# Kernel optimization log

Hardware: AMD Instinct MI355X
Metric: run time of the kernel (lower is better)

Reference implementation:

```python
import jax, jax.numpy as jnp
import numpy as np

B = 65536
N_SPARSE = 20
N_VARLEN = 3
SEQ_LEN = 50
VOCAB = 100000
N_DENSE = 13


def setup_inputs() -> dict:
    key = jax.random.key(0)
    k1, k2, k3, k4, k5, k6 = jax.random.split(key, 6)
    sparse_ids = jax.random.randint(k1, (B, N_SPARSE), 0, VOCAB, dtype=jnp.int64 if jax.config.jax_enable_x64 else jnp.int32)
    varlen_ids = jax.random.randint(k2, (B, N_VARLEN, SEQ_LEN), 0, VOCAB, dtype=sparse_ids.dtype)
    dense_x = jax.random.normal(k3, (B, N_DENSE), dtype=jnp.float32)
    # dim-1 embedding table per feature, stacked: [n_feat, vocab]
    sparse_tables = jax.random.normal(k4, (N_SPARSE, VOCAB), dtype=jnp.float32)
    varlen_tables = jax.random.normal(k5, (N_VARLEN, VOCAB), dtype=jnp.float32)
    dense_w = jax.random.normal(k6, (N_DENSE,), dtype=jnp.float32) * 1e-4
    return {
        "sparse_ids": sparse_ids,
        "varlen_ids": varlen_ids,
        "dense_x": dense_x,
        "sparse_tables": sparse_tables,
        "varlen_tables": varlen_tables,
        "dense_w": dense_w,
    }


def reference(sparse_ids, varlen_ids, dense_x, sparse_tables, varlen_tables, dense_w):
    # per-feature dim-1 embedding gather for single-value sparse feats: [B, Fs]
    fs = jnp.arange(N_SPARSE)
    sparse_vals = sparse_tables[fs[None, :], sparse_ids]
    # varlen gather: [B, Fv, L]; mask_zero=True -> id 0 contributes nothing; sum pooling
    fv = jnp.arange(N_VARLEN)
    varlen_vals = varlen_tables[fv[None, :, None], varlen_ids]
    mask = (varlen_ids != 0).astype(varlen_vals.dtype)
    varlen_pool = jnp.sum(varlen_vals * mask, axis=-1)  # [B, Fv]
    # reduce_sum over concat([sparse_vals, varlen_pool]) == sum of both sums
    logit = jnp.sum(sparse_vals, axis=-1) + jnp.sum(varlen_pool, axis=-1)
    # linear dense logit: concat(dense) @ W[:,1], squeezed
    logit = logit + dense_x @ dense_w
    return logit  # [B]
```

## Files before the change

kernel.cpp:

```cpp
#include <hip/hip_runtime.h>

constexpr int B        = 65536;
constexpr int N_SPARSE = 20;
constexpr int N_VARLEN = 3;
constexpr int SEQ_LEN  = 50;
constexpr int VOCAB    = 100000;
constexpr int N_DENSE  = 13;
constexpr int VAR_TOT  = N_VARLEN * SEQ_LEN;

typedef int   v4i __attribute__((ext_vector_type(4)));
typedef float v2f __attribute__((ext_vector_type(2)));

__global__ __launch_bounds__(256) void logit_kernel(
    const int*   __restrict__ sparse_ids,
    const int*   __restrict__ varlen_ids,
    const float* __restrict__ dense_x,
    const float* __restrict__ sparse_tables,
    const float* __restrict__ varlen_tables,
    const float* __restrict__ dense_w,
    float*       __restrict__ out)
{
    const int tid = blockIdx.x * blockDim.x + threadIdx.x;
    const int g   = tid >> 4;
    const int t   = tid & 15;

    const v4i* vptr = (const v4i*)varlen_ids + (long)g * 75;
    const v4i* sptr = (const v4i*)sparse_ids + (long)g * 10;
    const v2f* dptr = (const v2f*)dense_x    + (long)g * 13;

    v4i vid[5];
    #pragma unroll
    for (int k = 0; k < 4; ++k)
        vid[k] = __builtin_nontemporal_load(vptr + (t + 16 * k));
    vid[4] = __builtin_nontemporal_load(vptr + (t > 10 ? 74 : t + 64));
    const v4i sid = __builtin_nontemporal_load(sptr + (t > 9 ? 9 : t));
    const v2f dx  = __builtin_nontemporal_load(dptr + (t > 12 ? 12 : t));

    float vval[20];
    #pragma unroll
    for (int k = 0; k < 5; ++k) {
        const int c = (k == 4) ? (t + 64) : (t + 16 * k);
        #pragma unroll
        for (int j = 0; j < 4; ++j) {
            const int s = 4 * c + j;
            int p = (s >= VAR_TOT) ? (s - VAR_TOT) : s;
            p = (p > VAR_TOT - 1) ? (VAR_TOT - 1) : p;
            const int v = (p >= 100) ? 2 : (p >= 50 ? 1 : 0);
            vval[4 * k + j] = varlen_tables[v * VOCAB + vid[k][j]];
        }
    }
    float sval[4];
    {
        const int c = (t > 9) ? 9 : t;
        #pragma unroll
        for (int j = 0; j < 4; ++j) {
            const int s = 4 * c + j;
            const int f = (s >= N_SPARSE) ? (s - N_SPARSE) : s;
            sval[j] = sparse_tables[f * VOCAB + sid[j]];
        }
    }

    float acc0 = 0.f, acc1 = 0.f;

    #pragma unroll
    for (int k = 0; k < 5; ++k) {
        const int c = (k == 4) ? (t + 64) : (t + 16 * k);
        #pragma unroll
        for (int j = 0; j < 4; ++j) {
            const int s   = 4 * c + j;
            const bool ok = (s < 2 * VAR_TOT);
            const bool r1 = (s >= VAR_TOT);
            const float m = (ok && vid[k][j] != 0) ? vval[4 * k + j] : 0.f;
            acc0 += r1 ? 0.f : m;
            acc1 += r1 ? m   : 0.f;
        }
    }
    {
        const int c   = (t > 9) ? 9 : t;
        const bool ok = (t < 10);
        #pragma unroll
        for (int j = 0; j < 4; ++j) {
            const int s   = 4 * c + j;
            const bool r1 = (s >= N_SPARSE);
            const float m = ok ? sval[j] : 0.f;
            acc0 += r1 ? 0.f : m;
            acc1 += r1 ? m   : 0.f;
        }
    }
    {
        const int c   = (t > 12) ? 12 : t;
        const bool ok = (t < 13);
        #pragma unroll
        for (int j = 0; j < 2; ++j) {
            const int s   = 2 * c + j;
            const bool r1 = (s >= N_DENSE);
            const int d   = r1 ? (s - N_DENSE) : s;
            const float m = ok ? dx[j] * dense_w[d] : 0.f;
            acc0 += r1 ? 0.f : m;
            acc1 += r1 ? m   : 0.f;
        }
    }

    #pragma unroll
    for (int o = 1; o < 16; o <<= 1) {
        acc0 += __shfl_xor(acc0, o);
        acc1 += __shfl_xor(acc1, o);
    }
    if (t == 0) {
        v2f r = { acc0, acc1 };
        __builtin_nontemporal_store(r, (v2f*)out + g);
    }
}

extern "C" void kernel_launch(void* const* d_in, const int* in_sizes, int n_in,
                              void* d_out, int out_size, void* d_ws, size_t ws_size,
                              hipStream_t stream) {
    const int*   sparse_ids    = (const int*)d_in[0];
    const int*   varlen_ids    = (const int*)d_in[1];
    const float* dense_x       = (const float*)d_in[2];
    const float* sparse_tables = (const float*)d_in[3];
    const float* varlen_tables = (const float*)d_in[4];
    const float* dense_w       = (const float*)d_in[5];
    float*       out           = (float*)d_out;

    const int threads = 256;
    const int total   = (B / 2) * 16;
    const int blocks  = total / threads;
    logit_kernel<<<blocks, threads, 0, stream>>>(
        sparse_ids, varlen_ids, dense_x, sparse_tables, varlen_tables, dense_w, out);
}
```

Before: 144.3 us.

## Stage fp16 varlen tables through LDS in vocab slices instead of global gathers

```diff
diff --git a/kernel.cpp b/kernel.cpp
--- a/kernel.cpp
+++ b/kernel.cpp
@@ -8,47 +8,50 @@
 constexpr int N_DENSE  = 13;
 constexpr int VAR_TOT  = N_VARLEN * SEQ_LEN;
 
+constexpr int SLICE = 10000;
+constexpr int NPASS = VOCAB / SLICE;
+constexpr int LROW  = SLICE + 2;
+
 typedef int   v4i __attribute__((ext_vector_type(4)));
 typedef float v2f __attribute__((ext_vector_type(2)));
 
-__global__ __launch_bounds__(256) void logit_kernel(
+__global__ __launch_bounds__(512) void convert_kernel(
+    const float* __restrict__ vt, unsigned int* __restrict__ vt16)
+{
+    const int i = blockIdx.x * 512 + threadIdx.x;
+    if (i >= (N_VARLEN * VOCAB) / 2) return;
+    const v2f f = ((const v2f*)vt)[i];
+    const unsigned short lo = __builtin_bit_cast(unsigned short, (_Float16)f.x);
+    const unsigned short hi = __builtin_bit_cast(unsigned short, (_Float16)f.y);
+    vt16[i] = ((unsigned int)hi << 16) | lo;
+}
+
+__global__ __launch_bounds__(1024) void logit_kernel(
     const int*   __restrict__ sparse_ids,
     const int*   __restrict__ varlen_ids,
     const float* __restrict__ dense_x,
     const float* __restrict__ sparse_tables,
-    const float* __restrict__ varlen_tables,
     const float* __restrict__ dense_w,
+    const unsigned int* __restrict__ vt16,
     float*       __restrict__ out)
 {
-    const int tid = blockIdx.x * blockDim.x + threadIdx.x;
-    const int g   = tid >> 4;
-    const int t   = tid & 15;
+    __shared__ unsigned int ldsw[N_VARLEN * (LROW / 2)];
+    const unsigned short* lds16 = (const unsigned short*)ldsw;
+
+    const int tidb = threadIdx.x;
+    const int gtid = blockIdx.x * 1024 + tidb;
+    const int g    = gtid >> 4;
+    const int t    = gtid & 15;
 
     const v4i* vptr = (const v4i*)varlen_ids + (long)g * 75;
-    const v4i* sptr = (const v4i*)sparse_ids + (long)g * 10;
-    const v2f* dptr = (const v2f*)dense_x    + (long)g * 13;
-
     v4i vid[5];
     #pragma unroll
     for (int k = 0; k < 4; ++k)
         vid[k] = __builtin_nontemporal_load(vptr + (t + 16 * k));
     vid[4] = __builtin_nontemporal_load(vptr + (t > 10 ? 74 : t + 64));
-    const v4i sid = __builtin_nontemporal_load(sptr + (t > 9 ? 9 : t));
-    const v2f dx  = __builtin_nontemporal_load(dptr + (t > 12 ? 12 : t));
+    const v4i sid = __builtin_nontemporal_load((const v4i*)sparse_ids + (long)g * 10 + (t > 9 ? 9 : t));
+    const v2f dx  = __builtin_nontemporal_load((const v2f*)dense_x    + (long)g * 13 + (t > 12 ? 12 : t));
 
-    float vval[20];
-    #pragma unroll
-    for (int k = 0; k < 5; ++k) {
-        const int c = (k == 4) ? (t + 64) : (t + 16 * k);
-        #pragma unroll
-        for (int j = 0; j < 4; ++j) {
-            const int s = 4 * c + j;
-            int p = (s >= VAR_TOT) ? (s - VAR_TOT) : s;
-            p = (p > VAR_TOT - 1) ? (VAR_TOT - 1) : p;
-            const int v = (p >= 100) ? 2 : (p >= 50 ? 1 : 0);
-            vval[4 * k + j] = varlen_tables[v * VOCAB + vid[k][j]];
-        }
-    }
     float sval[4];
     {
         const int c = (t > 9) ? 9 : t;
@@ -60,8 +63,8 @@
         }
     }
 
-    float acc0 = 0.f, acc1 = 0.f;
-
+    int   vbase[20];
+    float wsgn[20];
     #pragma unroll
     for (int k = 0; k < 5; ++k) {
         const int c = (k == 4) ? (t + 64) : (t + 16 * k);
@@ -70,11 +73,49 @@
             const int s   = 4 * c + j;
             const bool ok = (s < 2 * VAR_TOT);
             const bool r1 = (s >= VAR_TOT);
-            const float m = (ok && vid[k][j] != 0) ? vval[4 * k + j] : 0.f;
-            acc0 += r1 ? 0.f : m;
-            acc1 += r1 ? m   : 0.f;
+            int p = r1 ? (s - VAR_TOT) : s;
+            p = (p > VAR_TOT - 1) ? (VAR_TOT - 1) : p;
+            const int v = (p >= 100) ? 2 : (p >= 50 ? 1 : 0);
+            vbase[4 * k + j] = v * LROW;
+            wsgn[4 * k + j]  = ok ? (r1 ? -1.f : 1.f) : 0.f;
         }
     }
+
+    float accS = 0.f, accD = 0.f;
+
+    for (int p = 0; p < NPASS; ++p) {
+        __syncthreads();
+        #pragma unroll
+        for (int v = 0; v < 3; ++v) {
+            const unsigned int* src = vt16 + v * (VOCAB / 2) + p * (SLICE / 2);
+            for (int k = tidb; k < SLICE / 2; k += 1024) {
+                unsigned int w = src[k];
+                if (p == 0 && k == 0) w &= 0xffff0000u;
+                ldsw[v * (LROW / 2) + k] = w;
+            }
+        }
+        if (tidb < 3) ldsw[tidb * (LROW / 2) + SLICE / 2] = 0;
+        __syncthreads();
+
+        const int lo = p * SLICE;
+        #pragma unroll
+        for (int k = 0; k < 5; ++k) {
+            #pragma unroll
+            for (int j = 0; j < 4; ++j) {
+                const int slot = 4 * k + j;
+                unsigned int off = (unsigned int)(vid[k][j] - lo);
+                off = (off > (unsigned)SLICE) ? (unsigned)SLICE : off;
+                const unsigned short raw = lds16[vbase[slot] + (int)off];
+                const float val = (float)__builtin_bit_cast(_Float16, raw);
+                accD += val * wsgn[slot];
+                accS += val * __builtin_fabsf(wsgn[slot]);
+            }
+        }
+    }
+
+    float acc0 = 0.5f * (accS + accD);
+    float acc1 = 0.5f * (accS - accD);
+
     {
         const int c   = (t > 9) ? 9 : t;
         const bool ok = (t < 10);
@@ -122,10 +163,11 @@
     const float* varlen_tables = (const float*)d_in[4];
     const float* dense_w       = (const float*)d_in[5];
     float*       out           = (float*)d_out;
+    unsigned int* vt16         = (unsigned int*)d_ws;
 
-    const int threads = 256;
-    const int total   = (B / 2) * 16;
-    const int blocks  = total / threads;
-    logit_kernel<<<blocks, threads, 0, stream>>>(
-        sparse_ids, varlen_ids, dense_x, sparse_tables, varlen_tables, dense_w, out);
+    const int nconv = (N_VARLEN * VOCAB) / 2;
+    convert_kernel<<<(nconv + 511) / 512, 512, 0, stream>>>(varlen_tables, vt16);
+
+    logit_kernel<<<(B / 2) / 64, 1024, 0, stream>>>(
+        sparse_ids, varlen_ids, dense_x, sparse_tables, dense_w, vt16, out);
 }
```

Measured after the change: 158.0 us. +9.5%, slower.
